# Kernel optimization log

Hardware: AMD Instinct MI355X
Metric: run time of the kernel (lower is better)

Reference implementation:

```python
import jax, jax.numpy as jnp
import numpy as np

N = 102400   # total nodes
F = 400      # node features
E = 1638400  # edges
H = 64       # hidden channels
L = 3        # num_layers (hidden convs); +1 final conv to width 1
K = 300      # sort-pool k
NPER = 400   # nodes per graph (uniform graphs)
B = N // NPER
D = H * L + 1  # total_latent_dim = 193


def setup_inputs() -> dict:
    key = jax.random.key(0)
    ks = jax.random.split(key, 20)
    def lin(k, i, o):
        return jax.random.normal(k, (i, o), jnp.float32) / np.sqrt(i)
    inp = {
        "x": jax.random.normal(ks[0], (N, F), jnp.float32),
        "edge_index": jax.random.randint(ks[1], (2, E), 0, N, jnp.int64),
        "W1": lin(ks[2], F, H), "b1": jnp.zeros((H,), jnp.float32),
        "W2": lin(ks[3], H, H), "b2": jnp.zeros((H,), jnp.float32),
        "W3": lin(ks[4], H, H), "b3": jnp.zeros((H,), jnp.float32),
        "W4": lin(ks[5], H, 1), "b4": jnp.zeros((1,), jnp.float32),
        "cw1": jax.random.normal(ks[6], (16, 1, D), jnp.float32) / np.sqrt(D),
        "cb1": jnp.zeros((16,), jnp.float32),
        "cw2": jax.random.normal(ks[7], (32, 16, 5), jnp.float32) / np.sqrt(16 * 5),
        "cb2": jnp.zeros((32,), jnp.float32),
        "mw1": lin(ks[8], 4672, 32), "mb1": jnp.zeros((32,), jnp.float32),
        "mw2": lin(ks[9], 32, 2), "mb2": jnp.zeros((2,), jnp.float32),
    }
    return inp


def _gcn(x, W, b, src, dst, norm):
    h = x @ W                                   # [N, out]
    msg = h[src] * norm[:, None]                # [E', out]
    out = jax.ops.segment_sum(msg, dst, num_segments=N)
    return out + b


def reference(x, edge_index, W1, b1, W2, b2, W3, b3, W4, b4,
              cw1, cb1, cw2, cb2, mw1, mb1, mw2, mb2):
    # GCN normalization with self-loops (D^-1/2 (A+I) D^-1/2)
    loops = jnp.arange(N, dtype=edge_index.dtype)
    src = jnp.concatenate([edge_index[0], loops])
    dst = jnp.concatenate([edge_index[1], loops])
    deg = jax.ops.segment_sum(jnp.ones_like(src, jnp.float32), dst, num_segments=N)
    dis = jax.lax.rsqrt(jnp.maximum(deg, 1.0))
    norm = dis[src] * dis[dst]

    h1 = jnp.tanh(_gcn(x, W1, b1, src, dst, norm))
    h2 = jnp.tanh(_gcn(h1, W2, b2, src, dst, norm))
    h3 = jnp.tanh(_gcn(h2, W3, b3, src, dst, norm))
    h4 = jnp.tanh(_gcn(h3, W4, b4, src, dst, norm))
    feat = jnp.concatenate([h1, h2, h3, h4], axis=-1)  # [N, D]

    # SortAggregation: per-graph sort by last channel (descending), take top-k
    fg = feat.reshape(B, NPER, D)
    order = jnp.argsort(-fg[:, :, -1], axis=1)[:, :K]  # [B, K]
    pooled = jnp.take_along_axis(fg, order[:, :, None], axis=1)  # [B, K, D]
    z = pooled.reshape(B, 1, K * D)

    dn = ("NCH", "OIH", "NCH")
    z = jax.lax.conv_general_dilated(z, cw1, (D,), "VALID", dimension_numbers=dn)
    z = jax.nn.relu(z + cb1[None, :, None])            # [B, 16, K]
    z = jax.lax.reduce_window(z, -jnp.inf, jax.lax.max, (1, 1, 2), (1, 1, 2), "VALID")
    z = jax.lax.conv_general_dilated(z, cw2, (1,), "VALID", dimension_numbers=dn)
    z = jax.nn.relu(z + cb2[None, :, None])            # [B, 32, 146]
    z = z.reshape(B, -1)                               # [B, 4672]
    z = jax.nn.relu(z @ mw1 + mb1)
    return z @ mw2 + mb2                               # [B, 2]
```

## Files before the change

### kernel.cpp

```cpp
#include <hip/hip_runtime.h>
#include <cstdint>
#include <cstddef>

#define Nn 102400
#define Ff 400
#define Ee 1638400
#define Kk 300
#define Bb 256
#define CAP 64

__device__ __forceinline__ float xla_tanhf(float x) {
    const float c = 7.90531110763549805f;
    float xc = fminf(fmaxf(x, -c), c);
    float x2 = __fmul_rn(xc, xc);
    float p = -2.76076847742355e-16f;
    p = __fadd_rn(__fmul_rn(p, x2),  2.00018790482477e-13f);
    p = __fadd_rn(__fmul_rn(p, x2), -8.60467152213735e-11f);
    p = __fadd_rn(__fmul_rn(p, x2),  5.12229709037114e-08f);
    p = __fadd_rn(__fmul_rn(p, x2),  1.48572235717979e-05f);
    p = __fadd_rn(__fmul_rn(p, x2),  6.37261928875436e-04f);
    p = __fadd_rn(__fmul_rn(p, x2),  4.89352455891786e-03f);
    p = __fmul_rn(p, xc);
    float q = 1.19825839466702e-06f;
    q = __fadd_rn(__fmul_rn(q, x2), 1.18534705686654e-04f);
    q = __fadd_rn(__fmul_rn(q, x2), 2.26843463243900e-03f);
    q = __fadd_rn(__fmul_rn(q, x2), 4.89352518554385e-03f);
    float r = __fdiv_rn(p, q);
    return (fabsf(x) < 0.0004f) ? x : r;
}

__global__ void scat_k(const int* __restrict__ ei, int* __restrict__ fill,
                       int* __restrict__ csr) {
    int e = blockIdx.x * 256 + threadIdx.x;
    if (e >= Ee) return;
    int d = ei[Ee + e];
    int p = atomicAdd(&fill[d], 1);
    if (p < CAP) csr[(size_t)d * CAP + p] = e;
}

__global__ __launch_bounds__(256) void sortrow_k(const int* __restrict__ ei,
                                                 const int* __restrict__ deg,
                                                 int* __restrict__ csr,
                                                 float* __restrict__ dis) {
    int lane = threadIdx.x & 63;
    int v = blockIdx.x * 4 + (threadIdx.x >> 6);
    int dvf = deg[v];
    int dv = min(dvf, CAP);
    if (lane == 0) dis[v] = 1.0f / sqrtf((float)(dvf + 1));
    int key = (lane < dv) ? csr[(size_t)v * CAP + lane] : 0x7FFFFFFF;
#pragma unroll
    for (int k = 2; k <= 64; k <<= 1) {
#pragma unroll
        for (int j = k >> 1; j; j >>= 1) {
            int other = __shfl_xor(key, j);
            bool up = ((lane & k) == 0);
            bool lower = ((lane & j) == 0);
            key = (lower == up) ? min(key, other) : max(key, other);
        }
    }
    if (lane < dv) csr[(size_t)v * CAP + lane] = ei[key];
}

template <int CH>
__global__ __launch_bounds__(64) void gemm_w32(const float* __restrict__ A,
                                               const float* __restrict__ B,
                                               float* __restrict__ C) {
    constexpr int K = 16 * CH;
    __shared__ __align__(16) float As[16 * 32];
    __shared__ __align__(16) float Bs[16][68];
    int tid = threadIdx.x;
    int tx = tid & 15;
    int ty = tid >> 4;
    int base = blockIdx.x * 32;
    int sr = tid >> 1, sh = tid & 1;
    int bk = tid >> 2, bn = (tid & 3) * 16;
    float acc[8][4] = {};
    for (int ch = 0; ch < CH; ++ch) {
        int k0 = ch * 16;
        const float* ap = A + (size_t)(base + sr) * K + k0 + sh * 8;
        float4 v0 = *(const float4*)(ap);
        float4 v1 = *(const float4*)(ap + 4);
        float a8[8] = {v0.x, v0.y, v0.z, v0.w, v1.x, v1.y, v1.z, v1.w};
        float4 bv4[4];
        const float* bp = B + (size_t)(k0 + bk) * 64 + bn;
#pragma unroll
        for (int q = 0; q < 4; ++q) bv4[q] = *(const float4*)(bp + q * 4);
        __syncthreads();
#pragma unroll
        for (int q = 0; q < 8; ++q) As[(sh * 8 + q) * 32 + sr] = a8[q];
#pragma unroll
        for (int q = 0; q < 4; ++q) *(float4*)&Bs[bk][bn + q * 4] = bv4[q];
        __syncthreads();
#pragma unroll
        for (int kk = 0; kk < 16; ++kk) {
            float4 f0 = *(const float4*)&As[kk * 32 + ty * 8];
            float4 f1 = *(const float4*)&As[kk * 32 + ty * 8 + 4];
            float av[8] = {f0.x, f0.y, f0.z, f0.w, f1.x, f1.y, f1.z, f1.w};
            float2 b01 = *(const float2*)&Bs[kk][tx * 2];
            float2 b23 = *(const float2*)&Bs[kk][32 + tx * 2];
            float bv[4] = {b01.x, b01.y, b23.x, b23.y};
#pragma unroll
            for (int r = 0; r < 8; ++r)
#pragma unroll
                for (int c = 0; c < 4; ++c) acc[r][c] = fmaf(av[r], bv[c], acc[r][c]);
        }
    }
#pragma unroll
    for (int r = 0; r < 8; ++r) {
        float* cp = C + (size_t)(base + ty * 8 + r) * 64;
        *(float2*)(cp + tx * 2)      = make_float2(acc[r][0], acc[r][1]);
        *(float2*)(cp + 32 + tx * 2) = make_float2(acc[r][2], acc[r][3]);
    }
}

__global__ __launch_bounds__(256) void agg64_k(const float* __restrict__ t,
                                               const float* __restrict__ bias,
                                               const float* __restrict__ dis,
                                               const int* __restrict__ deg,
                                               const int* __restrict__ csr,
                                               float* __restrict__ out,
                                               const float* __restrict__ W4,
                                               float* __restrict__ t4) {
    int lane = threadIdx.x & 63;
    int wv = __builtin_amdgcn_readfirstlane(threadIdx.x >> 6);
    int v = blockIdx.x * 4 + wv;
    int dv = min(deg[v], CAP);
    float dsv = dis[v];
    const int* row = csr + (size_t)v * CAP;
    float acc = 0.0f;
    int j = 0;
    for (; j + 16 <= dv; j += 16) {
        int u[16]; float d[16], tv[16];
#pragma unroll
        for (int q = 0; q < 16; ++q) u[q] = __builtin_amdgcn_readfirstlane(row[j + q]);
#pragma unroll
        for (int q = 0; q < 16; ++q) tv[q] = t[(size_t)u[q] * 64 + lane];
#pragma unroll
        for (int q = 0; q < 16; ++q) d[q] = dis[u[q]];
#pragma unroll
        for (int q = 0; q < 16; ++q)
            acc = __fadd_rn(acc, __fmul_rn(tv[q], __fmul_rn(d[q], dsv)));
    }
    for (; j + 4 <= dv; j += 4) {
        int u[4]; float d[4], tv[4];
#pragma unroll
        for (int q = 0; q < 4; ++q) u[q] = __builtin_amdgcn_readfirstlane(row[j + q]);
#pragma unroll
        for (int q = 0; q < 4; ++q) tv[q] = t[(size_t)u[q] * 64 + lane];
#pragma unroll
        for (int q = 0; q < 4; ++q) d[q] = dis[u[q]];
#pragma unroll
        for (int q = 0; q < 4; ++q)
            acc = __fadd_rn(acc, __fmul_rn(tv[q], __fmul_rn(d[q], dsv)));
    }
    for (; j < dv; ++j) {
        int u = __builtin_amdgcn_readfirstlane(row[j]);
        acc = __fadd_rn(acc, __fmul_rn(t[(size_t)u * 64 + lane], __fmul_rn(dis[u], dsv)));
    }
    acc = __fadd_rn(acc, __fmul_rn(t[(size_t)v * 64 + lane], __fmul_rn(dsv, dsv)));
    float res = xla_tanhf(__fadd_rn(acc, bias[lane]));
    out[(size_t)v * 64 + lane] = res;
    if (t4 != nullptr) {
        float w4l = W4[lane];
        float a4 = 0.0f;
#pragma unroll
        for (int k = 0; k < 64; ++k) {
            float hk = __shfl(res, k);
            float wk = __shfl(w4l, k);
            a4 = fmaf(hk, wk, a4);
        }
        if (lane == 0) t4[v] = a4;
    }
}

__global__ void agg1_k(const float* __restrict__ t4, const float* __restrict__ dis,
                       const int* __restrict__ deg, const int* __restrict__ csr,
                       const float* __restrict__ b4, float* __restrict__ h4) {
    int v = blockIdx.x * 256 + threadIdx.x;
    if (v >= Nn) return;
    int dv = min(deg[v], CAP);
    float dsv = dis[v];
    float acc = 0.0f;
    const int* row = csr + (size_t)v * CAP;
    for (int j = 0; j < dv; ++j) {
        int u = row[j];
        acc = __fadd_rn(acc, __fmul_rn(t4[u], __fmul_rn(dis[u], dsv)));
    }
    acc = __fadd_rn(acc, __fmul_rn(t4[v], __fmul_rn(dsv, dsv)));
    h4[v] = xla_tanhf(__fadd_rn(acc, b4[0]));
}

__global__ __launch_bounds__(512) void sort_k(const float* __restrict__ h4,
                                              int* __restrict__ order) {
    __shared__ unsigned int kv[512];
    __shared__ int ki[512];
    int tid = threadIdx.x, g = blockIdx.x;
    unsigned int key = 0xFFFFFFFFu;
    if (tid < 400) {
        unsigned int u = __float_as_uint(h4[g * 400 + tid]);
        u = (u & 0x80000000u) ? ~u : (u | 0x80000000u);
        key = ~u;
    }
    kv[tid] = key; ki[tid] = tid;
    __syncthreads();
    for (int size = 2; size <= 512; size <<= 1) {
        for (int stride = size >> 1; stride > 0; stride >>= 1) {
            int p = tid ^ stride;
            if (p > tid) {
                bool asc = ((tid & size) == 0);
                unsigned int a = kv[tid], b = kv[p];
                int ia = ki[tid], ib = ki[p];
                bool gt = (a > b) || (a == b && ia > ib);
                if (gt == asc) { kv[tid] = b; kv[p] = a; ki[tid] = ib; ki[p] = ia; }
            }
            __syncthreads();
        }
    }
    if (tid < Kk) order[g * Kk + tid] = ki[tid];
}

__global__ __launch_bounds__(128) void conv1_k(const float* __restrict__ h1,
                                               const float* __restrict__ h2,
                                               const float* __restrict__ h3,
                                               const float* __restrict__ h4,
                                               const int* __restrict__ order,
                                               const float* __restrict__ cw1,
                                               const float* __restrict__ cb1,
                                               float* __restrict__ z1) {
    __shared__ double wt[193 * 16];
    int tid = threadIdx.x, b = blockIdx.y;
    for (int i = tid; i < 193 * 16; i += 128) {
        int c = i / 193, d = i % 193;
        wt[d * 16 + c] = (double)cw1[i];
    }
    __syncthreads();
    int kpos = blockIdx.x * 128 + tid;
    if (kpos >= Kk) return;
    int n = b * 400 + order[b * Kk + kpos];
    double acc[16];
#pragma unroll
    for (int c = 0; c < 16; ++c) acc[c] = (double)cb1[c];
    const float* bases[3] = {h1 + (size_t)n * 64, h2 + (size_t)n * 64, h3 + (size_t)n * 64};
    for (int r = 0; r < 3; ++r) {
        const float* p = bases[r];
        for (int d = 0; d < 64; ++d) {
            double xv = (double)p[d];
            const double* wp = &wt[((size_t)r * 64 + d) * 16];
#pragma unroll
            for (int c = 0; c < 16; ++c) acc[c] += xv * wp[c];
        }
    }
    double xl = (double)h4[n];
    {
        const double* wp = &wt[192 * 16];
#pragma unroll
        for (int c = 0; c < 16; ++c) acc[c] += xl * wp[c];
    }
#pragma unroll
    for (int c = 0; c < 16; ++c)
        z1[((size_t)b * 16 + c) * 300 + kpos] = (float)fmax(acc[c], 0.0);
}

__global__ __launch_bounds__(256) void tail_k(const float* __restrict__ z1,
                                              const float* __restrict__ cw2,
                                              const float* __restrict__ cb2,
                                              const float* __restrict__ mw1,
                                              const float* __restrict__ mb1,
                                              const float* __restrict__ mw2,
                                              const float* __restrict__ mb2,
                                              float* __restrict__ out) {
    __shared__ float lz[16 * 150];
    __shared__ float lw[2560];
    __shared__ float lz3[4672];
    __shared__ double red[256];
    __shared__ double s4[32];
    int b = blockIdx.x, tid = threadIdx.x;
    for (int i = tid; i < 2400; i += 256) {
        int bc = i / 150, j = i % 150;
        const float* zp = z1 + ((size_t)b * 16 + bc) * 300 + 2 * j;
        lz[i] = fmaxf(zp[0], zp[1]);
    }
    for (int i = tid; i < 2560; i += 256) lw[i] = cw2[i];
    __syncthreads();
    for (int o = tid; o < 4672; o += 256) {
        int co = o / 146, j = o % 146;
        float acc = cb2[co];
#pragma unroll
        for (int ci = 0; ci < 16; ++ci)
#pragma unroll
            for (int tt = 0; tt < 5; ++tt)
                acc += lz[ci * 150 + j + tt] * lw[co * 80 + ci * 5 + tt];
        lz3[o] = fmaxf(acc, 0.f);
    }
    __syncthreads();
    int o = tid & 31, part = tid >> 5;
    double acc = 0.0;
    for (int i = part * 584; i < (part + 1) * 584; ++i)
        acc += (double)lz3[i] * (double)mw1[(size_t)i * 32 + o];
    red[tid] = acc;
    __syncthreads();
    if (tid < 32) {
        double s = 0.0;
#pragma unroll
        for (int p = 0; p < 8; ++p) s += red[p * 32 + tid];
        s4[tid] = fmax(s + (double)mb1[tid], 0.0);
    }
    __syncthreads();
    if (tid < 2) {
        double s = (double)mb2[tid];
#pragma unroll
        for (int j = 0; j < 32; ++j) s += s4[j] * (double)mw2[j * 2 + tid];
        out[b * 2 + tid] = (float)s;
    }
}

extern "C" void kernel_launch(void* const* d_in, const int* in_sizes, int n_in,
                              void* d_out, int out_size, void* d_ws, size_t ws_size,
                              hipStream_t stream) {
    const float* x   = (const float*)d_in[0];
    const int*   ei  = (const int*)d_in[1];
    const float* W1  = (const float*)d_in[2];  const float* b1  = (const float*)d_in[3];
    const float* W2  = (const float*)d_in[4];  const float* b2  = (const float*)d_in[5];
    const float* W3  = (const float*)d_in[6];  const float* b3  = (const float*)d_in[7];
    const float* W4  = (const float*)d_in[8];  const float* b4  = (const float*)d_in[9];
    const float* cw1 = (const float*)d_in[10]; const float* cb1 = (const float*)d_in[11];
    const float* cw2 = (const float*)d_in[12]; const float* cb2 = (const float*)d_in[13];
    const float* mw1 = (const float*)d_in[14]; const float* mb1 = (const float*)d_in[15];
    const float* mw2 = (const float*)d_in[16]; const float* mb2 = (const float*)d_in[17];
    float* out = (float*)d_out;

    const size_t N64 = (size_t)Nn * 64;
    float* t   = (float*)d_ws;
    float* h1  = t + N64;
    float* h2  = h1 + N64;
    float* h3  = h2 + N64;
    float* t4  = h3 + N64;
    float* h4  = t4 + Nn;
    float* dis = h4 + Nn;
    int*   fill = (int*)(dis + Nn);
    int*   csr  = fill + Nn;
    int*   order = csr + (size_t)Nn * CAP;
    float* z1 = (float*)t;

    hipMemsetAsync(fill, 0, sizeof(int) * (size_t)Nn, stream);

    scat_k<<<Ee / 256, 256, 0, stream>>>(ei, fill, csr);
    sortrow_k<<<Nn / 4, 256, 0, stream>>>(ei, fill, csr, dis);

    gemm_w32<25><<<Nn / 32, 64, 0, stream>>>(x, W1, t);
    agg64_k<<<Nn / 4, 256, 0, stream>>>(t, b1, dis, fill, csr, h1, nullptr, nullptr);
    gemm_w32<4> <<<Nn / 32, 64, 0, stream>>>(h1, W2, t);
    agg64_k<<<Nn / 4, 256, 0, stream>>>(t, b2, dis, fill, csr, h2, nullptr, nullptr);
    gemm_w32<4> <<<Nn / 32, 64, 0, stream>>>(h2, W3, t);
    agg64_k<<<Nn / 4, 256, 0, stream>>>(t, b3, dis, fill, csr, h3, W4, t4);

    agg1_k<<<Nn / 256, 256, 0, stream>>>(t4, dis, fill, csr, b4, h4);

    sort_k<<<Bb, 512, 0, stream>>>(h4, order);
    conv1_k<<<dim3(3, Bb), 128, 0, stream>>>(h1, h2, h3, h4, order, cw1, cb1, z1);
    tail_k<<<Bb, 256, 0, stream>>>(z1, cw2, cb2, mw1, mb1, mw2, mb2, out);
}
```

Measured before the change: 1.138 ms.

## Fuse edge scatter with first GEMM, double-buffer GEMMs, precompute edge norms

The edge-scatter kernel and the first x@W1 GEMM are merged into one launch. Of every 9 blocks, one computes GEMM tiles and eight scatter edges, so the atomics can overlap with the compute. The fill counters are padded to one per 16 ints to cut atomic contention. GEMMs now run four independent waves per block with register double-buffering and no block-level syncs. Aggregation loads the CSR row once per wave and broadcasts indices with shuffles. Per-edge norms are precomputed in the first layer and reused by later layers, which adds an N*64 float buffer and extra memory traffic.

```diff
diff --git a/kernel.cpp b/kernel.cpp
--- a/kernel.cpp
+++ b/kernel.cpp
@@ -29,24 +29,124 @@
     return (fabsf(x) < 0.0004f) ? x : r;
 }
 
-__global__ void scat_k(const int* __restrict__ ei, int* __restrict__ fill,
-                       int* __restrict__ csr) {
-    int e = blockIdx.x * 256 + threadIdx.x;
-    if (e >= Ee) return;
-    int d = ei[Ee + e];
-    int p = atomicAdd(&fill[d], 1);
-    if (p < CAP) csr[(size_t)d * CAP + p] = e;
+template <int CH>
+__device__ __forceinline__ void gemm_wave(const float* __restrict__ A,
+                                          const float* __restrict__ B,
+                                          float* __restrict__ C,
+                                          int tile, int tid,
+                                          float* __restrict__ Asw,
+                                          float* __restrict__ Bsw) {
+    constexpr int K = 16 * CH;
+    int tx = tid & 15;
+    int ty = tid >> 4;
+    int base = tile * 32;
+    int sr = tid >> 1, sh = tid & 1;
+    int bk = tid >> 2, bn = (tid & 3) * 16;
+    const float* aip = A + (size_t)(base + sr) * K + sh * 8;
+    const float* bip = B + (size_t)bk * 64 + bn;
+    float acc[8][4] = {};
+    float4 aA0, aA1, aB0, aB1;
+    float4 bA[4], bB[4];
+    auto LOADG = [&](int ch, float4& a0, float4& a1, float4 (&bv)[4]) {
+        const float* ap = aip + ch * 16;
+        a0 = *(const float4*)(ap);
+        a1 = *(const float4*)(ap + 4);
+        const float* bp = bip + (size_t)ch * 16 * 64;
+        bv[0] = *(const float4*)(bp);
+        bv[1] = *(const float4*)(bp + 4);
+        bv[2] = *(const float4*)(bp + 8);
+        bv[3] = *(const float4*)(bp + 12);
+    };
+    auto STORE = [&](const float4& a0, const float4& a1, const float4 (&bv)[4]) {
+        Asw[(sh * 8 + 0) * 32 + sr] = a0.x;
+        Asw[(sh * 8 + 1) * 32 + sr] = a0.y;
+        Asw[(sh * 8 + 2) * 32 + sr] = a0.z;
+        Asw[(sh * 8 + 3) * 32 + sr] = a0.w;
+        Asw[(sh * 8 + 4) * 32 + sr] = a1.x;
+        Asw[(sh * 8 + 5) * 32 + sr] = a1.y;
+        Asw[(sh * 8 + 6) * 32 + sr] = a1.z;
+        Asw[(sh * 8 + 7) * 32 + sr] = a1.w;
+        *(float4*)&Bsw[bk * 68 + bn]      = bv[0];
+        *(float4*)&Bsw[bk * 68 + bn + 4]  = bv[1];
+        *(float4*)&Bsw[bk * 68 + bn + 8]  = bv[2];
+        *(float4*)&Bsw[bk * 68 + bn + 12] = bv[3];
+    };
+    auto COMPUTE = [&]() {
+#pragma unroll
+        for (int kk = 0; kk < 16; ++kk) {
+            float4 f0 = *(const float4*)&Asw[kk * 32 + ty * 8];
+            float4 f1 = *(const float4*)&Asw[kk * 32 + ty * 8 + 4];
+            float2 b01 = *(const float2*)&Bsw[kk * 68 + tx * 2];
+            float2 b23 = *(const float2*)&Bsw[kk * 68 + 32 + tx * 2];
+            float av[8] = {f0.x, f0.y, f0.z, f0.w, f1.x, f1.y, f1.z, f1.w};
+            float bv2[4] = {b01.x, b01.y, b23.x, b23.y};
+#pragma unroll
+            for (int r = 0; r < 8; ++r)
+#pragma unroll
+                for (int c = 0; c < 4; ++c) acc[r][c] = fmaf(av[r], bv2[c], acc[r][c]);
+        }
+    };
+    LOADG(0, aA0, aA1, bA);
+    int ch = 0;
+    while (true) {
+        STORE(aA0, aA1, bA);
+        if (ch + 1 < CH) LOADG(ch + 1, aB0, aB1, bB);
+        COMPUTE();
+        if (++ch >= CH) break;
+        STORE(aB0, aB1, bB);
+        if (ch + 1 < CH) LOADG(ch + 1, aA0, aA1, bA);
+        COMPUTE();
+        if (++ch >= CH) break;
+    }
+#pragma unroll
+    for (int r = 0; r < 8; ++r) {
+        float* cp = C + (size_t)(base + ty * 8 + r) * 64;
+        *(float2*)(cp + tx * 2)      = make_float2(acc[r][0], acc[r][1]);
+        *(float2*)(cp + 32 + tx * 2) = make_float2(acc[r][2], acc[r][3]);
+    }
+}
+
+template <int CH>
+__global__ __launch_bounds__(256) void gemm_k(const float* __restrict__ A,
+                                              const float* __restrict__ B,
+                                              float* __restrict__ C) {
+    __shared__ __align__(16) float As[4][16 * 32];
+    __shared__ __align__(16) float Bs[4][16 * 68];
+    int wid = threadIdx.x >> 6, tid = threadIdx.x & 63;
+    gemm_wave<CH>(A, B, C, blockIdx.x * 4 + wid, tid, As[wid], Bs[wid]);
+}
+
+__global__ __launch_bounds__(256) void fat_k(const int* __restrict__ ei,
+                                             int* __restrict__ fill,
+                                             int* __restrict__ csr,
+                                             const float* __restrict__ x,
+                                             const float* __restrict__ W1,
+                                             float* __restrict__ t) {
+    __shared__ __align__(16) float As[4][16 * 32];
+    __shared__ __align__(16) float Bs[4][16 * 68];
+    int b = blockIdx.x;
+    int g = b / 9, r = b - g * 9;
+    if (r == 0) {
+        int wid = threadIdx.x >> 6, tid = threadIdx.x & 63;
+        gemm_wave<25>(x, W1, t, g * 4 + wid, tid, As[wid], Bs[wid]);
+    } else {
+        int e = (g * 8 + (r - 1)) * 256 + threadIdx.x;
+        int d = ei[Ee + e];
+        int p = atomicAdd(&fill[(size_t)d * 16], 1);
+        if (p < CAP) csr[(size_t)d * CAP + p] = e;
+    }
 }
 
 __global__ __launch_bounds__(256) void sortrow_k(const int* __restrict__ ei,
-                                                 const int* __restrict__ deg,
+                                                 const int* __restrict__ fill,
                                                  int* __restrict__ csr,
-                                                 float* __restrict__ dis) {
+                                                 float* __restrict__ dis,
+                                                 int* __restrict__ degc) {
     int lane = threadIdx.x & 63;
     int v = blockIdx.x * 4 + (threadIdx.x >> 6);
-    int dvf = deg[v];
+    int dvf = fill[(size_t)v * 16];
     int dv = min(dvf, CAP);
-    if (lane == 0) dis[v] = 1.0f / sqrtf((float)(dvf + 1));
+    if (lane == 0) { dis[v] = 1.0f / sqrtf((float)(dvf + 1)); degc[v] = dvf; }
     int key = (lane < dv) ? csr[(size_t)v * CAP + lane] : 0x7FFFFFFF;
 #pragma unroll
     for (int k = 2; k <= 64; k <<= 1) {
@@ -61,106 +161,63 @@
     if (lane < dv) csr[(size_t)v * CAP + lane] = ei[key];
 }
 
-template <int CH>
-__global__ __launch_bounds__(64) void gemm_w32(const float* __restrict__ A,
-                                               const float* __restrict__ B,
-                                               float* __restrict__ C) {
-    constexpr int K = 16 * CH;
-    __shared__ __align__(16) float As[16 * 32];
-    __shared__ __align__(16) float Bs[16][68];
-    int tid = threadIdx.x;
-    int tx = tid & 15;
-    int ty = tid >> 4;
-    int base = blockIdx.x * 32;
-    int sr = tid >> 1, sh = tid & 1;
-    int bk = tid >> 2, bn = (tid & 3) * 16;
-    float acc[8][4] = {};
-    for (int ch = 0; ch < CH; ++ch) {
-        int k0 = ch * 16;
-        const float* ap = A + (size_t)(base + sr) * K + k0 + sh * 8;
-        float4 v0 = *(const float4*)(ap);
-        float4 v1 = *(const float4*)(ap + 4);
-        float a8[8] = {v0.x, v0.y, v0.z, v0.w, v1.x, v1.y, v1.z, v1.w};
-        float4 bv4[4];
-        const float* bp = B + (size_t)(k0 + bk) * 64 + bn;
-#pragma unroll
-        for (int q = 0; q < 4; ++q) bv4[q] = *(const float4*)(bp + q * 4);
-        __syncthreads();
-#pragma unroll
-        for (int q = 0; q < 8; ++q) As[(sh * 8 + q) * 32 + sr] = a8[q];
-#pragma unroll
-        for (int q = 0; q < 4; ++q) *(float4*)&Bs[bk][bn + q * 4] = bv4[q];
-        __syncthreads();
-#pragma unroll
-        for (int kk = 0; kk < 16; ++kk) {
-            float4 f0 = *(const float4*)&As[kk * 32 + ty * 8];
-            float4 f1 = *(const float4*)&As[kk * 32 + ty * 8 + 4];
-            float av[8] = {f0.x, f0.y, f0.z, f0.w, f1.x, f1.y, f1.z, f1.w};
-            float2 b01 = *(const float2*)&Bs[kk][tx * 2];
-            float2 b23 = *(const float2*)&Bs[kk][32 + tx * 2];
-            float bv[4] = {b01.x, b01.y, b23.x, b23.y};
-#pragma unroll
-            for (int r = 0; r < 8; ++r)
-#pragma unroll
-                for (int c = 0; c < 4; ++c) acc[r][c] = fmaf(av[r], bv[c], acc[r][c]);
-        }
-    }
-#pragma unroll
-    for (int r = 0; r < 8; ++r) {
-        float* cp = C + (size_t)(base + ty * 8 + r) * 64;
-        *(float2*)(cp + tx * 2)      = make_float2(acc[r][0], acc[r][1]);
-        *(float2*)(cp + 32 + tx * 2) = make_float2(acc[r][2], acc[r][3]);
-    }
-}
-
-__global__ __launch_bounds__(256) void agg64_k(const float* __restrict__ t,
-                                               const float* __restrict__ bias,
-                                               const float* __restrict__ dis,
-                                               const int* __restrict__ deg,
-                                               const int* __restrict__ csr,
-                                               float* __restrict__ out,
-                                               const float* __restrict__ W4,
-                                               float* __restrict__ t4) {
+template <int PHASE>
+__global__ __launch_bounds__(256, 4) void agg64_k(const float* __restrict__ t,
+                                                  const float* __restrict__ bias,
+                                                  const float* __restrict__ dis,
+                                                  const int* __restrict__ degc,
+                                                  const int* __restrict__ csr,
+                                                  float* __restrict__ nrm,
+                                                  float* __restrict__ out,
+                                                  const float* __restrict__ W4,
+                                                  float* __restrict__ t4) {
     int lane = threadIdx.x & 63;
     int wv = __builtin_amdgcn_readfirstlane(threadIdx.x >> 6);
     int v = blockIdx.x * 4 + wv;
-    int dv = min(deg[v], CAP);
+    int dv = __builtin_amdgcn_readfirstlane(min(degc[v], CAP));
     float dsv = dis[v];
-    const int* row = csr + (size_t)v * CAP;
+    float tself = t[(size_t)v * 64 + lane];
+    float bsl = bias[lane];
+    int idxl = (lane < dv) ? csr[(size_t)v * CAP + lane] : v;
+    float nr;
+    if (PHASE == 1) {
+        nr = __fmul_rn(dis[idxl], dsv);
+        nrm[(size_t)v * 64 + lane] = nr;
+    } else {
+        nr = nrm[(size_t)v * 64 + lane];
+    }
     float acc = 0.0f;
     int j = 0;
     for (; j + 16 <= dv; j += 16) {
-        int u[16]; float d[16], tv[16];
-#pragma unroll
-        for (int q = 0; q < 16; ++q) u[q] = __builtin_amdgcn_readfirstlane(row[j + q]);
-#pragma unroll
-        for (int q = 0; q < 16; ++q) tv[q] = t[(size_t)u[q] * 64 + lane];
-#pragma unroll
-        for (int q = 0; q < 16; ++q) d[q] = dis[u[q]];
+        float tv[16];
+#pragma unroll
+        for (int q = 0; q < 16; ++q) {
+            int u = __builtin_amdgcn_readfirstlane(__shfl(idxl, j + q));
+            tv[q] = t[(size_t)u * 64 + lane];
+        }
 #pragma unroll
         for (int q = 0; q < 16; ++q)
-            acc = __fadd_rn(acc, __fmul_rn(tv[q], __fmul_rn(d[q], dsv)));
+            acc = __fadd_rn(acc, __fmul_rn(tv[q], __shfl(nr, j + q)));
     }
     for (; j + 4 <= dv; j += 4) {
-        int u[4]; float d[4], tv[4];
-#pragma unroll
-        for (int q = 0; q < 4; ++q) u[q] = __builtin_amdgcn_readfirstlane(row[j + q]);
-#pragma unroll
-        for (int q = 0; q < 4; ++q) tv[q] = t[(size_t)u[q] * 64 + lane];
-#pragma unroll
-        for (int q = 0; q < 4; ++q) d[q] = dis[u[q]];
+        float tv[4];
+#pragma unroll
+        for (int q = 0; q < 4; ++q) {
+            int u = __builtin_amdgcn_readfirstlane(__shfl(idxl, j + q));
+            tv[q] = t[(size_t)u * 64 + lane];
+        }
 #pragma unroll
         for (int q = 0; q < 4; ++q)
-            acc = __fadd_rn(acc, __fmul_rn(tv[q], __fmul_rn(d[q], dsv)));
+            acc = __fadd_rn(acc, __fmul_rn(tv[q], __shfl(nr, j + q)));
     }
     for (; j < dv; ++j) {
-        int u = __builtin_amdgcn_readfirstlane(row[j]);
-        acc = __fadd_rn(acc, __fmul_rn(t[(size_t)u * 64 + lane], __fmul_rn(dis[u], dsv)));
-    }
-    acc = __fadd_rn(acc, __fmul_rn(t[(size_t)v * 64 + lane], __fmul_rn(dsv, dsv)));
-    float res = xla_tanhf(__fadd_rn(acc, bias[lane]));
+        int u = __builtin_amdgcn_readfirstlane(__shfl(idxl, j));
+        acc = __fadd_rn(acc, __fmul_rn(t[(size_t)u * 64 + lane], __shfl(nr, j)));
+    }
+    acc = __fadd_rn(acc, __fmul_rn(tself, __fmul_rn(dsv, dsv)));
+    float res = xla_tanhf(__fadd_rn(acc, bsl));
     out[(size_t)v * 64 + lane] = res;
-    if (t4 != nullptr) {
+    if (W4 != nullptr) {
         float w4l = W4[lane];
         float a4 = 0.0f;
 #pragma unroll
@@ -174,18 +231,43 @@
 }
 
 __global__ void agg1_k(const float* __restrict__ t4, const float* __restrict__ dis,
-                       const int* __restrict__ deg, const int* __restrict__ csr,
+                       const int* __restrict__ degc, const int* __restrict__ csr,
+                       const float* __restrict__ nrm,
                        const float* __restrict__ b4, float* __restrict__ h4) {
     int v = blockIdx.x * 256 + threadIdx.x;
     if (v >= Nn) return;
-    int dv = min(deg[v], CAP);
+    int dv = min(degc[v], CAP);
     float dsv = dis[v];
+    const int* row = csr + (size_t)v * CAP;
+    const float* nr = nrm + (size_t)v * 64;
     float acc = 0.0f;
-    const int* row = csr + (size_t)v * CAP;
-    for (int j = 0; j < dv; ++j) {
-        int u = row[j];
-        acc = __fadd_rn(acc, __fmul_rn(t4[u], __fmul_rn(dis[u], dsv)));
-    }
+    int j = 0;
+    for (; j + 16 <= dv; j += 16) {
+        int u[16]; float nv[16], tv[16];
+#pragma unroll
+        for (int q = 0; q < 16; ++q) nv[q] = nr[j + q];
+#pragma unroll
+        for (int q = 0; q < 16; ++q) u[q] = row[j + q];
+#pragma unroll
+        for (int q = 0; q < 16; ++q) tv[q] = t4[u[q]];
+#pragma unroll
+        for (int q = 0; q < 16; ++q)
+            acc = __fadd_rn(acc, __fmul_rn(tv[q], nv[q]));
+    }
+    for (; j + 4 <= dv; j += 4) {
+        int u[4]; float nv[4], tv[4];
+#pragma unroll
+        for (int q = 0; q < 4; ++q) nv[q] = nr[j + q];
+#pragma unroll
+        for (int q = 0; q < 4; ++q) u[q] = row[j + q];
+#pragma unroll
+        for (int q = 0; q < 4; ++q) tv[q] = t4[u[q]];
+#pragma unroll
+        for (int q = 0; q < 4; ++q)
+            acc = __fadd_rn(acc, __fmul_rn(tv[q], nv[q]));
+    }
+    for (; j < dv; ++j)
+        acc = __fadd_rn(acc, __fmul_rn(t4[row[j]], nr[j]));
     acc = __fadd_rn(acc, __fmul_rn(t4[v], __fmul_rn(dsv, dsv)));
     h4[v] = xla_tanhf(__fadd_rn(acc, b4[0]));
 }
@@ -330,31 +412,32 @@
     float* out = (float*)d_out;
 
     const size_t N64 = (size_t)Nn * 64;
-    float* t   = (float*)d_ws;
-    float* h1  = t + N64;
-    float* h2  = h1 + N64;
-    float* h3  = h2 + N64;
-    float* t4  = h3 + N64;
-    float* h4  = t4 + Nn;
-    float* dis = h4 + Nn;
-    int*   fill = (int*)(dis + Nn);
-    int*   csr  = fill + Nn;
-    int*   order = csr + (size_t)Nn * CAP;
+    float* t    = (float*)d_ws;
+    float* h1   = t + N64;
+    float* h2   = h1 + N64;
+    float* h3   = h2 + N64;
+    float* t4   = h3 + N64;
+    float* h4   = t4 + Nn;
+    float* dis  = h4 + Nn;
+    int*   degc = (int*)(dis + Nn);
+    int*   fill = degc + Nn;
+    int*   csr  = fill + (size_t)Nn * 16;
+    float* nrm  = (float*)(csr + (size_t)Nn * CAP);
+    int*   order = (int*)(nrm + N64);
     float* z1 = (float*)t;
 
-    hipMemsetAsync(fill, 0, sizeof(int) * (size_t)Nn, stream);
-
-    scat_k<<<Ee / 256, 256, 0, stream>>>(ei, fill, csr);
-    sortrow_k<<<Nn / 4, 256, 0, stream>>>(ei, fill, csr, dis);
-
-    gemm_w32<25><<<Nn / 32, 64, 0, stream>>>(x, W1, t);
-    agg64_k<<<Nn / 4, 256, 0, stream>>>(t, b1, dis, fill, csr, h1, nullptr, nullptr);
-    gemm_w32<4> <<<Nn / 32, 64, 0, stream>>>(h1, W2, t);
-    agg64_k<<<Nn / 4, 256, 0, stream>>>(t, b2, dis, fill, csr, h2, nullptr, nullptr);
-    gemm_w32<4> <<<Nn / 32, 64, 0, stream>>>(h2, W3, t);
-    agg64_k<<<Nn / 4, 256, 0, stream>>>(t, b3, dis, fill, csr, h3, W4, t4);
-
-    agg1_k<<<Nn / 256, 256, 0, stream>>>(t4, dis, fill, csr, b4, h4);
+    hipMemsetAsync(fill, 0, sizeof(int) * (size_t)Nn * 16, stream);
+
+    fat_k<<<7200, 256, 0, stream>>>(ei, fill, csr, x, W1, t);
+    sortrow_k<<<Nn / 4, 256, 0, stream>>>(ei, fill, csr, dis, degc);
+
+    agg64_k<1><<<Nn / 4, 256, 0, stream>>>(t, b1, dis, degc, csr, nrm, h1, nullptr, nullptr);
+    gemm_k<4><<<Nn / 32 / 4, 256, 0, stream>>>(h1, W2, t);
+    agg64_k<0><<<Nn / 4, 256, 0, stream>>>(t, b2, dis, degc, csr, nrm, h2, nullptr, nullptr);
+    gemm_k<4><<<Nn / 32 / 4, 256, 0, stream>>>(h2, W3, t);
+    agg64_k<0><<<Nn / 4, 256, 0, stream>>>(t, b3, dis, degc, csr, nrm, h3, W4, t4);
+
+    agg1_k<<<Nn / 256, 256, 0, stream>>>(t4, dis, degc, csr, nrm, b4, h4);
 
     sort_k<<<Bb, 512, 0, stream>>>(h4, order);
     conv1_k<<<dim3(3, Bb), 128, 0, stream>>>(h1, h2, h3, h4, order, cw1, cb1, z1);
```

Result: faster. 1.115 ms (-2.0%).
